# Kernel optimization log

Hardware: AMD Instinct MI355X
Metric: run time of the kernel (lower is better)

Reference implementation:

```python
import jax, jax.numpy as jnp
import numpy as np

N = {'QENT': 20000, 'CENT': 50000, 'SPAN': 40000, 'SENT': 40000}
E = 250000
IN_DIM, HID = 256, 128
NEG_SLOPE = 0.2  # GATConv default negative_slope
RELS = [('QENT', 'SPAN'), ('QENT', 'SENT'), ('CENT', 'SENT'), ('SPAN', 'CENT'), ('CENT', 'CENT')]
ENAMES = ['e_qent_span', 'e_qent_sent', 'e_cent_sent', 'e_span_cent', 'e_cent_cooccur']


def setup_inputs() -> dict:
    key = jax.random.key(0)
    ks = jax.random.split(key, 20)
    inp = {}
    for i, t in enumerate(['QENT', 'CENT', 'SPAN', 'SENT']):
        inp['x_' + t] = jax.random.normal(ks[i], (N[t], IN_DIM), jnp.float32)
    for i, (nm, (s, d)) in enumerate(zip(ENAMES, RELS)):
        k1, k2 = jax.random.split(ks[4 + i])
        src = jax.random.randint(k1, (E,), 0, N[s])
        dst = jax.random.randint(k2, (E,), 0, N[d])
        inp[nm] = jnp.stack([src, dst]).astype(jnp.int32)
    inp['lin_W'] = jax.random.normal(ks[10], (4, IN_DIM, HID), jnp.float32) / np.sqrt(IN_DIM).astype(np.float32)
    inp['lin_b'] = jnp.zeros((4, HID), jnp.float32)
    inp['conv_Ws'] = jax.random.normal(ks[11], (2, 5, HID, HID), jnp.float32) / np.sqrt(HID).astype(np.float32)
    inp['conv_Wd'] = jax.random.normal(ks[12], (2, 5, HID, HID), jnp.float32) / np.sqrt(HID).astype(np.float32)
    inp['conv_as'] = jax.random.normal(ks[13], (2, 5, HID), jnp.float32) / np.sqrt(HID).astype(np.float32)
    inp['conv_ad'] = jax.random.normal(ks[14], (2, 5, HID), jnp.float32) / np.sqrt(HID).astype(np.float32)
    inp['conv_b'] = jnp.zeros((2, 5, HID), jnp.float32)
    inp['out_W'] = jax.random.normal(ks[15], (HID, 1), jnp.float32) / np.sqrt(HID).astype(np.float32)
    inp['out_b'] = jnp.zeros((1,), jnp.float32)
    return inp


def _gat(x_src, x_dst, edge, Ws, Wd, a_s, a_d, b, n_dst):
    """PyG GATConv, heads=1, concat=True, add_self_loops=False, bipartite lin_src/lin_dst."""
    hs = x_src @ Ws                       # [Ns, H]
    hd = x_dst @ Wd                       # [Nd, H]
    src, dst = edge[0], edge[1]
    e = jax.nn.leaky_relu((hs @ a_s)[src] + (hd @ a_d)[dst], NEG_SLOPE)  # [E]
    m = jax.ops.segment_max(e, dst, num_segments=n_dst)
    m = jnp.where(jnp.isfinite(m), m, 0.0)
    ex = jnp.exp(e - m[dst])
    denom = jax.ops.segment_sum(ex, dst, num_segments=n_dst)
    alpha = ex / (denom[dst] + 1e-16)     # segment softmax (PyG adds 1e-16)
    out = jax.ops.segment_sum(alpha[:, None] * hs[src], dst, num_segments=n_dst)
    return out + b


def _forward(x_QENT, x_CENT, x_SPAN, x_SENT,
             e_qent_span, e_qent_sent, e_cent_sent, e_span_cent, e_cent_cooccur,
             lin_W, lin_b, conv_Ws, conv_Wd, conv_as, conv_ad, conv_b, out_W, out_b):
    # per-type input projection (pyg Linear has bias)
    x = {'QENT': x_QENT @ lin_W[0] + lin_b[0],
         'CENT': x_CENT @ lin_W[1] + lin_b[1],
         'SPAN': x_SPAN @ lin_W[2] + lin_b[2],
         'SENT': x_SENT @ lin_W[3] + lin_b[3]}
    for l in range(2):
        p = lambda r: (conv_Ws[l, r], conv_Wd[l, r], conv_as[l, r], conv_ad[l, r], conv_b[l, r])
        span = _gat(x['QENT'], x['SPAN'], e_qent_span, *p(0), N['SPAN'])
        sent = (_gat(x['QENT'], x['SENT'], e_qent_sent, *p(1), N['SENT'])
                + _gat(x['CENT'], x['SENT'], e_cent_sent, *p(2), N['SENT']))  # HeteroConv aggr='sum'
        cent = (_gat(x['SPAN'], x['CENT'], e_span_cent, *p(3), N['CENT'])
                + _gat(x['CENT'], x['CENT'], e_cent_cooccur, *p(4), N['CENT']))
        x = {'QENT': x['QENT'],  # QENT has no incoming edges; carried through so layer 2 can use it as source
             'SPAN': jax.nn.relu(span),
             'SENT': jax.nn.relu(sent),
             'CENT': jax.nn.relu(cent)}
    return (x['SPAN'] @ out_W + out_b)[:, 0]  # squeeze(-1) -> [N_SPAN]


def reference(x_QENT, x_CENT, x_SPAN, x_SENT,
              e_qent_span, e_qent_sent, e_cent_sent, e_span_cent, e_cent_cooccur,
              lin_W, lin_b, conv_Ws, conv_Wd, conv_as, conv_ad, conv_b, out_W, out_b):
    return _forward(x_QENT, x_CENT, x_SPAN, x_SENT,
                    e_qent_span, e_qent_sent, e_cent_sent, e_span_cent, e_cent_cooccur,
                    lin_W, lin_b, conv_Ws, conv_Wd, conv_as, conv_ad, conv_b, out_W, out_b)
```

## Files before the change

### kernel.cpp

```cpp
#include <hip/hip_runtime.h>
#include <hip/hip_fp16.h>

#define IN_DIM 256
#define HID 128
#define ELLW 16
#define OVF_CAP 32768

using bf16x8 = __attribute__((ext_vector_type(8))) short;
using f32x4 = __attribute__((ext_vector_type(4))) float;

struct h8 { __half2 a, b, c, d; };

__device__ __forceinline__ unsigned short f2bf(float f) {
    unsigned u = __float_as_uint(f);
    u += 0x7fffu + ((u >> 16) & 1u);
    return (unsigned short)(u >> 16);
}

template <int CTRL>
__device__ __forceinline__ float dpp_rot(float x) {
    return __int_as_float(
        __builtin_amdgcn_update_dpp(0, __float_as_int(x), CTRL, 0xf, 0xf, false));
}
__device__ __forceinline__ float rsum16(float x) {
    x += dpp_rot<0x121>(x);
    x += dpp_rot<0x122>(x);
    x += dpp_rot<0x124>(x);
    x += dpp_rot<0x128>(x);
    return x;
}
__device__ __forceinline__ float rmax16(float x) {
    x = fmaxf(x, dpp_rot<0x121>(x));
    x = fmaxf(x, dpp_rot<0x122>(x));
    x = fmaxf(x, dpp_rot<0x124>(x));
    x = fmaxf(x, dpp_rot<0x128>(x));
    return x;
}

__device__ __forceinline__ float lrelu(float t) { return t > 0.f ? t : 0.2f * t; }

__device__ __forceinline__ void accum8(f32x4& a0, f32x4& a1, float a, const h8& hv) {
    const float2 f0 = __half22float2(hv.a);
    const float2 f1 = __half22float2(hv.b);
    const float2 f2 = __half22float2(hv.c);
    const float2 f3 = __half22float2(hv.d);
    a0[0] += a * f0.x; a0[1] += a * f0.y;
    a0[2] += a * f1.x; a0[3] += a * f1.y;
    a1[0] += a * f2.x; a1[1] += a * f2.y;
    a1[2] += a * f3.x; a1[3] += a * f3.y;
}

__device__ __forceinline__ float epilogue16(const f32x4& a0, const f32x4& a1,
                                            const float* __restrict__ bias,
                                            const float* __restrict__ dvec, int sl) {
    const f32x4 bb0 = *reinterpret_cast<const f32x4*>(bias + sl * 8);
    const f32x4 bb1 = *reinterpret_cast<const f32x4*>(bias + sl * 8 + 4);
    const f32x4 d0 = *reinterpret_cast<const f32x4*>(dvec + sl * 8);
    const f32x4 d1 = *reinterpret_cast<const f32x4*>(dvec + sl * 8 + 4);
    float q = 0.f;
#pragma unroll
    for (int i = 0; i < 4; ++i) {
        q += fmaxf(a0[i] + bb0[i], 0.f) * d0[i];
        q += fmaxf(a1[i] + bb1[i], 0.f) * d1[i];
    }
    return rsum16(q);
}

__global__ __launch_bounds__(256) void setup_k(const float* __restrict__ lin_W,
                                               const float* __restrict__ lin_b,
                                               const float* __restrict__ conv_Ws,
                                               const float* __restrict__ Wd,
                                               const float* __restrict__ adv,
                                               short* __restrict__ wt0,
                                               short* __restrict__ wt1,
                                               float* __restrict__ bc,
                                               float* __restrict__ wd_out,
                                               float* __restrict__ v2,
                                               float* __restrict__ c2,
                                               int* __restrict__ deg,
                                               int* __restrict__ ovf_cnt, int NS) {
    const int b = blockIdx.x;
    if (b < 256) {
        const int idx = b * 256 + threadIdx.x;
        const int l = idx >> 15;
        const int rem = idx & 32767;
        const int k = rem >> 7;
        const int n = rem & 127;
        const float* lw = lin_W + (size_t)k * HID;
        const float* cw = conv_Ws + (size_t)(l * 5) * HID * HID + n;
        float s = 0.f;
#pragma unroll 4
        for (int m = 0; m < HID; ++m) s += lw[m] * cw[(size_t)m * HID];
        short* wt = l ? wt1 : wt0;
        wt[((k >> 3) << 10) + (n << 3) + (k & 7)] = (short)f2bf(s);
    } else if (b == 256) {
        const int t = threadIdx.x;
        const int l = t >> 7;
        const int n = t & 127;
        const float* cw = conv_Ws + (size_t)(l * 5) * HID * HID + n;
        float s = 0.f;
#pragma unroll 4
        for (int m = 0; m < HID; ++m) s += lin_b[m] * cw[(size_t)m * HID];
        bc[t] = s;
        if (t == 0) ovf_cnt[0] = 0;
    } else if (b == 257) {
        __shared__ float wd1s[HID];
        const int t = threadIdx.x;
        const int l = t >> 7, j = t & 127;
        const float* w = Wd + ((size_t)(l * 5) * HID + j) * HID;
        const float* a = adv + (size_t)(l * 5) * HID;
        float s = 0.f;
        for (int k = 0; k < HID; k += 4) {
            const float4 wv = *reinterpret_cast<const float4*>(w + k);
            const float4 av = *reinterpret_cast<const float4*>(a + k);
            s += wv.x * av.x + wv.y * av.y + wv.z * av.z + wv.w * av.w;
        }
        wd_out[t] = s;
        if (l == 0) wd1s[j] = s;
        __syncthreads();
        const float* wr = lin_W + 2 * (size_t)IN_DIM * HID + (size_t)t * HID;
        float p = 0.f;
        for (int k = 0; k < HID; k += 4) {
            const float4 wv = *reinterpret_cast<const float4*>(wr + k);
            p += wv.x * wd1s[k] + wv.y * wd1s[k + 1] + wv.z * wd1s[k + 2] +
                 wv.w * wd1s[k + 3];
        }
        v2[t] = p;
        if (t == 0) {
            const float* br = lin_b + 2 * HID;
            float q = 0.f;
            for (int k = 0; k < HID; ++k) q += br[k] * wd1s[k];
            c2[0] = q;
        }
    } else {
        const int i4 = ((b - 258) * 256 + threadIdx.x) * 4;
        if (i4 + 4 <= NS) {
            *reinterpret_cast<int4*>(deg + i4) = make_int4(0, 0, 0, 0);
        } else {
            for (int i = i4; i < NS; ++i) deg[i] = 0;
        }
    }
}

__global__ __launch_bounds__(256) void build_gemm_k(
    const int* __restrict__ src, const int* __restrict__ dst, int E,
    int* __restrict__ deg, int* __restrict__ ell, int2* __restrict__ ovf,
    int* __restrict__ ovf_cnt, const float* __restrict__ A,
    const short* __restrict__ Wt0, const short* __restrict__ Wt1,
    const float* __restrict__ bc, __half* __restrict__ hs,
    float2* __restrict__ as12, const float* __restrict__ a1v,
    const float* __restrict__ a2v, int N, int eb,
    const float* __restrict__ x_span, const float* __restrict__ v2,
    const float* __restrict__ c2, float* __restrict__ ad1_out, int NS, int gb) {
    if ((int)blockIdx.x < eb) {
        const int e = blockIdx.x * 256 + threadIdx.x;
        if (e < E) {
            const int d = dst[e], s = src[e];
            const int pos = atomicAdd(deg + d, 1);
            if (pos < ELLW) {
                ell[(size_t)d * ELLW + pos] = s;
            } else {
                const int oi = atomicAdd(ovf_cnt, 1);
                if (oi < OVF_CAP) ovf[oi] = make_int2(d, s);
            }
        }
        return;
    }
    if ((int)blockIdx.x >= eb + gb) {
        const int idx = ((int)blockIdx.x - eb - gb) * 256 + threadIdx.x;
        const int row = idx >> 4;
        const int sl = threadIdx.x & 15;
        if (row >= NS) return;
        const float* xr = x_span + (size_t)row * IN_DIM + sl * 16;
        const float* vr = v2 + sl * 16;
        float p = 0.f;
#pragma unroll
        for (int i = 0; i < 4; ++i) {
            const float4 xv = *reinterpret_cast<const float4*>(xr + i * 4);
            const float4 vv = *reinterpret_cast<const float4*>(vr + i * 4);
            p += xv.x * vv.x + xv.y * vv.y + xv.z * vv.z + xv.w * vv.w;
        }
        p = rsum16(p);
        if (sl == 0) ad1_out[row] = p + c2[0];
        return;
    }
    const int bid = (int)blockIdx.x - eb;
    const int tid = threadIdx.x;
    const int w = tid >> 6;
    const int lane = tid & 63;
    const int m16 = lane & 15;
    const int kg = lane >> 4;

    const int arow = bid * 64 + w * 16 + m16;
    const bool ok = arow < N;

    f32x4 acc[16];
#pragma unroll
    for (int j = 0; j < 16; ++j) acc[j] = (f32x4){0.f, 0.f, 0.f, 0.f};

    for (int k0 = 0; k0 < IN_DIM; k0 += 32) {
        bf16x8 af = {0, 0, 0, 0, 0, 0, 0, 0};
        if (ok) {
            const float* ap = A + (size_t)arow * IN_DIM + k0 + kg * 8;
            const float4 f0 = *reinterpret_cast<const float4*>(ap);
            const float4 f1 = *reinterpret_cast<const float4*>(ap + 4);
            af[0] = (short)f2bf(f0.x); af[1] = (short)f2bf(f0.y);
            af[2] = (short)f2bf(f0.z); af[3] = (short)f2bf(f0.w);
            af[4] = (short)f2bf(f1.x); af[5] = (short)f2bf(f1.y);
            af[6] = (short)f2bf(f1.z); af[7] = (short)f2bf(f1.w);
        }
        const int boff = ((k0 >> 3) + kg) << 10;
        const short* b0 = Wt0 + boff;
        const short* b1 = Wt1 + boff;
#pragma unroll
        for (int j = 0; j < 8; ++j) {
            const bf16x8 bf0 = *reinterpret_cast<const bf16x8*>(b0 + ((j * 16 + m16) << 3));
            acc[j] = __builtin_amdgcn_mfma_f32_16x16x32_bf16(af, bf0, acc[j], 0, 0, 0);
            const bf16x8 bf1 = *reinterpret_cast<const bf16x8*>(b1 + ((j * 16 + m16) << 3));
            acc[j + 8] = __builtin_amdgcn_mfma_f32_16x16x32_bf16(af, bf1, acc[j + 8], 0, 0, 0);
        }
    }

    const int rbase = bid * 64 + w * 16 + kg * 4;
    float p1[4] = {0.f, 0.f, 0.f, 0.f};
    float p2[4] = {0.f, 0.f, 0.f, 0.f};
#pragma unroll
    for (int j = 0; j < 8; ++j) {
        const int col = j * 16 + m16;
        const float b0v = bc[col];
        const float b1v = bc[128 + col];
        const float a1 = a1v[col];
        const float a2 = a2v[col];
        const int so = j * 32 + ((m16 >> 3) << 4) + (m16 & 7);
#pragma unroll
        for (int r = 0; r < 4; ++r) {
            const int row = rbase + r;
            const float v1 = acc[j][r] + b0v;
            const float v2v = acc[j + 8][r] + b1v;
            if (row < N) {
                hs[(size_t)row * 256 + so] = __float2half(v1);
                hs[(size_t)row * 256 + so + 8] = __float2half(v2v);
            }
            p1[r] += v1 * a1;
            p2[r] += v2v * a2;
        }
    }
#pragma unroll
    for (int r = 0; r < 4; ++r) {
        p1[r] = rsum16(p1[r]);
        p2[r] = rsum16(p2[r]);
    }
    if (m16 == 0)
#pragma unroll
        for (int r = 0; r < 4; ++r) {
            const int row = rbase + r;
            if (row < N) as12[row] = make_float2(p1[r], p2[r]);
        }
}

__global__ __launch_bounds__(256, 4) void gat_fused_k(
    const int* __restrict__ deg_arr, const int* __restrict__ ell,
    const int2* __restrict__ ovf, const int* __restrict__ ovf_cnt_p,
    const float* __restrict__ ad1_arr, const float2* __restrict__ as12,
    const __half* __restrict__ hs, const float* __restrict__ b1,
    const float* __restrict__ wd2v, const float* __restrict__ b2,
    const float* __restrict__ outW, const float* __restrict__ outb,
    float* __restrict__ out, int Ndst) {
    const int row = (blockIdx.x * blockDim.x + threadIdx.x) >> 6;
    const int lane = threadIdx.x & 63;
    const int sl = lane & 15;
    const int eg = lane >> 4;
    if (row >= Ndst) return;

    const int deg = deg_arr[row];
    int ce = ell[(size_t)row * ELLW + sl];
    if (sl >= deg) ce = 0;
    const float2 asv = as12[ce];
    const float ad1 = ad1_arr[row];

    if (deg <= ELLW) {
        const float ex1 = (sl < deg) ? __expf(lrelu(asv.x + ad1)) : 0.f;
        const float al1 = ex1 / (rsum16(ex1) + 1e-16f);

        f32x4 a0 = {0.f, 0.f, 0.f, 0.f}, a1 = {0.f, 0.f, 0.f, 0.f};
        h8 h2s[4];
#pragma unroll
        for (int r = 0; r < 4; ++r) {
            if (r * 4 < deg) {
                const int e = r * 4 + eg;
                const int s = __shfl(ce, e, 64);
                const float a = __shfl(al1, e, 64);
                const __half* hb = hs + (size_t)s * 256 + sl * 16;
                const h8 hv1 = *reinterpret_cast<const h8*>(hb);
                h2s[r] = *reinterpret_cast<const h8*>(hb + 8);
                accum8(a0, a1, a, hv1);
            }
        }
#pragma unroll
        for (int i = 0; i < 4; ++i) {
            a0[i] += __shfl_xor(a0[i], 16, 64);
            a0[i] += __shfl_xor(a0[i], 32, 64);
            a1[i] += __shfl_xor(a1[i], 16, 64);
            a1[i] += __shfl_xor(a1[i], 32, 64);
        }
        const float ad2 = epilogue16(a0, a1, b1, wd2v, sl);

        const float ex2 = (sl < deg) ? __expf(lrelu(asv.y + ad2)) : 0.f;
        const float al2 = ex2 / (rsum16(ex2) + 1e-16f);

        f32x4 b0 = {0.f, 0.f, 0.f, 0.f}, b1v = {0.f, 0.f, 0.f, 0.f};
#pragma unroll
        for (int r = 0; r < 4; ++r) {
            if (r * 4 < deg) {
                const float a = __shfl(al2, r * 4 + eg, 64);
                accum8(b0, b1v, a, h2s[r]);
            }
        }
#pragma unroll
        for (int i = 0; i < 4; ++i) {
            b0[i] += __shfl_xor(b0[i], 16, 64);
            b0[i] += __shfl_xor(b0[i], 32, 64);
            b1v[i] += __shfl_xor(b1v[i], 16, 64);
            b1v[i] += __shfl_xor(b1v[i], 32, 64);
        }
        const float q = epilogue16(b0, b1v, b2, outW, sl);
        if (lane == 0) out[row] = q + outb[0];
    } else {
        int oc = *ovf_cnt_p;
        if (oc > OVF_CAP) oc = OVF_CAP;
        float ad = ad1;
#pragma unroll
        for (int layer = 0; layer < 2; ++layer) {
            const float ac = layer ? asv.y : asv.x;
            const int ho = layer ? 8 : 0;
            const float* bias = layer ? b2 : b1;
            const float* dvec = layer ? outW : wd2v;

            float te = lrelu(ac + ad);
            float m = rmax16(te);
            for (int i = 0; i < oc; ++i) {
                const int2 o = ovf[i];
                if (o.x == row) {
                    const float2 oas = as12[o.y];
                    m = fmaxf(m, lrelu((layer ? oas.y : oas.x) + ad));
                }
            }
            const float ex = __expf(te - m);
            float dsum = rsum16(ex);
            for (int i = 0; i < oc; ++i) {
                const int2 o = ovf[i];
                if (o.x == row) {
                    const float2 oas = as12[o.y];
                    dsum += __expf(lrelu((layer ? oas.y : oas.x) + ad) - m);
                }
            }
            const float inv = 1.f / (dsum + 1e-16f);
            const float al = ex * inv;

            f32x4 acc0 = {0.f, 0.f, 0.f, 0.f}, acc1 = {0.f, 0.f, 0.f, 0.f};
            for (int i = 0; i < 16; ++i) {
                const int s = __shfl(ce, i, 64);
                float a = __shfl(al, i, 64);
                if (eg != 0) a = 0.f;
                const h8 hv =
                    *reinterpret_cast<const h8*>(hs + (size_t)s * 256 + sl * 16 + ho);
                accum8(acc0, acc1, a, hv);
            }
            for (int i = 0; i < oc; ++i) {
                const int2 o = ovf[i];
                if (o.x == row && eg == 0) {
                    const float2 oas = as12[o.y];
                    const float a = __expf(lrelu((layer ? oas.y : oas.x) + ad) - m) * inv;
                    const h8 hv =
                        *reinterpret_cast<const h8*>(hs + (size_t)o.y * 256 + sl * 16 + ho);
                    accum8(acc0, acc1, a, hv);
                }
            }
#pragma unroll
            for (int i = 0; i < 4; ++i) {
                acc0[i] += __shfl_xor(acc0[i], 16, 64);
                acc0[i] += __shfl_xor(acc0[i], 32, 64);
                acc1[i] += __shfl_xor(acc1[i], 16, 64);
                acc1[i] += __shfl_xor(acc1[i], 32, 64);
            }
            const float q = epilogue16(acc0, acc1, bias, dvec, sl);
            if (layer == 0) {
                ad = q;
            } else if (lane == 0) {
                out[row] = q + outb[0];
            }
        }
    }
}

extern "C" void kernel_launch(void* const* d_in, const int* in_sizes, int n_in,
                              void* d_out, int out_size, void* d_ws, size_t ws_size,
                              hipStream_t stream) {
    const float* x_qent = (const float*)d_in[0];
    const float* x_span = (const float*)d_in[2];
    const int* e_qs = (const int*)d_in[4];
    const float* lin_W = (const float*)d_in[9];
    const float* lin_b = (const float*)d_in[10];
    const float* conv_Ws = (const float*)d_in[11];
    const float* conv_Wd = (const float*)d_in[12];
    const float* conv_as = (const float*)d_in[13];
    const float* conv_ad = (const float*)d_in[14];
    const float* conv_b = (const float*)d_in[15];
    const float* out_W = (const float*)d_in[16];
    const float* out_b = (const float*)d_in[17];

    const int NQ = in_sizes[0] / IN_DIM;
    const int NS = in_sizes[2] / IN_DIM;
    const int E = in_sizes[4] / 2;
    const int* srcp = e_qs;
    const int* dstp = e_qs + E;
    (void)n_in; (void)out_size;

    float* ws = (float*)d_ws;
    size_t off = 0;
    auto alloc = [&](size_t n) {
        n = (n + 3) & ~(size_t)3;
        float* p = ws + off;
        off += n;
        return p;
    };
    __half* hs = (__half*)alloc((size_t)NQ * 128);
    float2* as12 = (float2*)alloc(2 * (size_t)NQ);
    float* ad1 = alloc(NS);
    float* wd2 = alloc(2 * HID);
    float* v2 = alloc(IN_DIM);
    float* c2 = alloc(1);
    float* bc = alloc(2 * HID);
    int* deg = (int*)alloc(NS);
    int* ell = (int*)alloc((size_t)NS * ELLW);
    int2* ovf = (int2*)alloc(2 * OVF_CAP);
    int* ovf_cnt = (int*)alloc(1);
    short* wt0 = (short*)alloc(IN_DIM * HID / 2);
    short* wt1 = (short*)alloc(IN_DIM * HID / 2);
    (void)ws_size;

    const int zd = (NS + 1023) / 1024;
    setup_k<<<dim3(258 + zd), dim3(256), 0, stream>>>(
        lin_W, lin_b, conv_Ws, conv_Wd, conv_ad, wt0, wt1, bc, wd2, v2, c2, deg, ovf_cnt,
        NS);

    const int eb = (E + 255) / 256;
    const int gb = (NQ + 63) / 64;
    const int ab = ((size_t)NS * 16 + 255) / 256;
    build_gemm_k<<<dim3(eb + gb + ab), dim3(256), 0, stream>>>(
        srcp, dstp, E, deg, ell, ovf, ovf_cnt, x_qent, wt0, wt1, bc, hs, as12, conv_as,
        conv_as + 5 * (size_t)HID, NQ, eb, x_span, v2, c2, ad1, NS, gb);

    gat_fused_k<<<dim3(((size_t)NS * 64 + 255) / 256), dim3(256), 0, stream>>>(
        deg, ell, ovf, ovf_cnt, ad1, as12, hs, conv_b, wd2 + HID,
        conv_b + 5 * (size_t)HID, out_W, out_b, (float*)d_out, NS);
}
```

Measured before the change: 85.60 us.

## Split GEMM blocks per weight matrix and reorder fused-kernel block roles

Each GEMM block previously computed both 128-wide projections (16 accumulators). It now computes one projection, selected by block-index parity, which doubles the GEMM block count and halves the accumulator registers per block. The block order inside the fused kernel also changes so GEMM blocks launch first, then the ad1 dot-product blocks, then the edge-scatter blocks, so the heavy work starts early. The trade-off is that each A row is read and converted to bf16 twice, and the two halves of the attention-score pair are now written by separate blocks as scalar stores.

```diff
diff --git a/kernel.cpp b/kernel.cpp
--- a/kernel.cpp
+++ b/kernel.cpp
@@ -148,26 +148,78 @@
     int* __restrict__ ovf_cnt, const float* __restrict__ A,
     const short* __restrict__ Wt0, const short* __restrict__ Wt1,
     const float* __restrict__ bc, __half* __restrict__ hs,
-    float2* __restrict__ as12, const float* __restrict__ a1v,
-    const float* __restrict__ a2v, int N, int eb,
+    float* __restrict__ as12,
+    const float* __restrict__ a1v, const float* __restrict__ a2v, int N,
     const float* __restrict__ x_span, const float* __restrict__ v2,
-    const float* __restrict__ c2, float* __restrict__ ad1_out, int NS, int gb) {
-    if ((int)blockIdx.x < eb) {
-        const int e = blockIdx.x * 256 + threadIdx.x;
-        if (e < E) {
-            const int d = dst[e], s = src[e];
-            const int pos = atomicAdd(deg + d, 1);
-            if (pos < ELLW) {
-                ell[(size_t)d * ELLW + pos] = s;
-            } else {
-                const int oi = atomicAdd(ovf_cnt, 1);
-                if (oi < OVF_CAP) ovf[oi] = make_int2(d, s);
-            }
-        }
+    const float* __restrict__ c2, float* __restrict__ ad1_out, int NS, int gb2,
+    int ab) {
+    const int b = (int)blockIdx.x;
+    if (b < gb2) {
+        const int l = b & 1;
+        const int bid = b >> 1;
+        const short* Wt = l ? Wt1 : Wt0;
+        const float* av = l ? a2v : a1v;
+        const int tid = threadIdx.x;
+        const int w = tid >> 6;
+        const int lane = tid & 63;
+        const int m16 = lane & 15;
+        const int kg = lane >> 4;
+
+        const int arow = bid * 64 + w * 16 + m16;
+        const bool ok = arow < N;
+
+        f32x4 acc[8];
+#pragma unroll
+        for (int j = 0; j < 8; ++j) acc[j] = (f32x4){0.f, 0.f, 0.f, 0.f};
+
+        for (int k0 = 0; k0 < IN_DIM; k0 += 32) {
+            bf16x8 af = {0, 0, 0, 0, 0, 0, 0, 0};
+            if (ok) {
+                const float* ap = A + (size_t)arow * IN_DIM + k0 + kg * 8;
+                const float4 f0 = *reinterpret_cast<const float4*>(ap);
+                const float4 f1 = *reinterpret_cast<const float4*>(ap + 4);
+                af[0] = (short)f2bf(f0.x); af[1] = (short)f2bf(f0.y);
+                af[2] = (short)f2bf(f0.z); af[3] = (short)f2bf(f0.w);
+                af[4] = (short)f2bf(f1.x); af[5] = (short)f2bf(f1.y);
+                af[6] = (short)f2bf(f1.z); af[7] = (short)f2bf(f1.w);
+            }
+            const short* bbase = Wt + (((k0 >> 3) + kg) << 10);
+#pragma unroll
+            for (int j = 0; j < 8; ++j) {
+                const bf16x8 bf =
+                    *reinterpret_cast<const bf16x8*>(bbase + ((j * 16 + m16) << 3));
+                acc[j] = __builtin_amdgcn_mfma_f32_16x16x32_bf16(af, bf, acc[j], 0, 0, 0);
+            }
+        }
+
+        const int rbase = bid * 64 + w * 16 + kg * 4;
+        float p[4] = {0.f, 0.f, 0.f, 0.f};
+#pragma unroll
+        for (int j = 0; j < 8; ++j) {
+            const int col = j * 16 + m16;
+            const float bv = bc[l * 128 + col];
+            const float a = av[col];
+            const int so = j * 32 + ((m16 >> 3) << 4) + (m16 & 7) + l * 8;
+#pragma unroll
+            for (int r = 0; r < 4; ++r) {
+                const int row = rbase + r;
+                const float v = acc[j][r] + bv;
+                if (row < N) hs[(size_t)row * 256 + so] = __float2half(v);
+                p[r] += v * a;
+            }
+        }
+#pragma unroll
+        for (int r = 0; r < 4; ++r) p[r] = rsum16(p[r]);
+        if (m16 == 0)
+#pragma unroll
+            for (int r = 0; r < 4; ++r) {
+                const int row = rbase + r;
+                if (row < N) as12[2 * (size_t)row + l] = p[r];
+            }
         return;
     }
-    if ((int)blockIdx.x >= eb + gb) {
-        const int idx = ((int)blockIdx.x - eb - gb) * 256 + threadIdx.x;
+    if (b < gb2 + ab) {
+        const int idx = (b - gb2) * 256 + threadIdx.x;
         const int row = idx >> 4;
         const int sl = threadIdx.x & 15;
         if (row >= NS) return;
@@ -184,78 +236,17 @@
         if (sl == 0) ad1_out[row] = p + c2[0];
         return;
     }
-    const int bid = (int)blockIdx.x - eb;
-    const int tid = threadIdx.x;
-    const int w = tid >> 6;
-    const int lane = tid & 63;
-    const int m16 = lane & 15;
-    const int kg = lane >> 4;
-
-    const int arow = bid * 64 + w * 16 + m16;
-    const bool ok = arow < N;
-
-    f32x4 acc[16];
-#pragma unroll
-    for (int j = 0; j < 16; ++j) acc[j] = (f32x4){0.f, 0.f, 0.f, 0.f};
-
-    for (int k0 = 0; k0 < IN_DIM; k0 += 32) {
-        bf16x8 af = {0, 0, 0, 0, 0, 0, 0, 0};
-        if (ok) {
-            const float* ap = A + (size_t)arow * IN_DIM + k0 + kg * 8;
-            const float4 f0 = *reinterpret_cast<const float4*>(ap);
-            const float4 f1 = *reinterpret_cast<const float4*>(ap + 4);
-            af[0] = (short)f2bf(f0.x); af[1] = (short)f2bf(f0.y);
-            af[2] = (short)f2bf(f0.z); af[3] = (short)f2bf(f0.w);
-            af[4] = (short)f2bf(f1.x); af[5] = (short)f2bf(f1.y);
-            af[6] = (short)f2bf(f1.z); af[7] = (short)f2bf(f1.w);
-        }
-        const int boff = ((k0 >> 3) + kg) << 10;
-        const short* b0 = Wt0 + boff;
-        const short* b1 = Wt1 + boff;
-#pragma unroll
-        for (int j = 0; j < 8; ++j) {
-            const bf16x8 bf0 = *reinterpret_cast<const bf16x8*>(b0 + ((j * 16 + m16) << 3));
-            acc[j] = __builtin_amdgcn_mfma_f32_16x16x32_bf16(af, bf0, acc[j], 0, 0, 0);
-            const bf16x8 bf1 = *reinterpret_cast<const bf16x8*>(b1 + ((j * 16 + m16) << 3));
-            acc[j + 8] = __builtin_amdgcn_mfma_f32_16x16x32_bf16(af, bf1, acc[j + 8], 0, 0, 0);
-        }
-    }
-
-    const int rbase = bid * 64 + w * 16 + kg * 4;
-    float p1[4] = {0.f, 0.f, 0.f, 0.f};
-    float p2[4] = {0.f, 0.f, 0.f, 0.f};
-#pragma unroll
-    for (int j = 0; j < 8; ++j) {
-        const int col = j * 16 + m16;
-        const float b0v = bc[col];
-        const float b1v = bc[128 + col];
-        const float a1 = a1v[col];
-        const float a2 = a2v[col];
-        const int so = j * 32 + ((m16 >> 3) << 4) + (m16 & 7);
-#pragma unroll
-        for (int r = 0; r < 4; ++r) {
-            const int row = rbase + r;
-            const float v1 = acc[j][r] + b0v;
-            const float v2v = acc[j + 8][r] + b1v;
-            if (row < N) {
-                hs[(size_t)row * 256 + so] = __float2half(v1);
-                hs[(size_t)row * 256 + so + 8] = __float2half(v2v);
-            }
-            p1[r] += v1 * a1;
-            p2[r] += v2v * a2;
-        }
-    }
-#pragma unroll
-    for (int r = 0; r < 4; ++r) {
-        p1[r] = rsum16(p1[r]);
-        p2[r] = rsum16(p2[r]);
-    }
-    if (m16 == 0)
-#pragma unroll
-        for (int r = 0; r < 4; ++r) {
-            const int row = rbase + r;
-            if (row < N) as12[row] = make_float2(p1[r], p2[r]);
-        }
+    const int e = (b - gb2 - ab) * 256 + threadIdx.x;
+    if (e < E) {
+        const int d = dst[e], s = src[e];
+        const int pos = atomicAdd(deg + d, 1);
+        if (pos < ELLW) {
+            ell[(size_t)d * ELLW + pos] = s;
+        } else {
+            const int oi = atomicAdd(ovf_cnt, 1);
+            if (oi < OVF_CAP) ovf[oi] = make_int2(d, s);
+        }
+    }
 }
 
 __global__ __launch_bounds__(256, 4) void gat_fused_k(
@@ -425,7 +416,7 @@
         return p;
     };
     __half* hs = (__half*)alloc((size_t)NQ * 128);
-    float2* as12 = (float2*)alloc(2 * (size_t)NQ);
+    float* as12 = alloc(2 * (size_t)NQ);
     float* ad1 = alloc(NS);
     float* wd2 = alloc(2 * HID);
     float* v2 = alloc(IN_DIM);
@@ -444,14 +435,14 @@
         lin_W, lin_b, conv_Ws, conv_Wd, conv_ad, wt0, wt1, bc, wd2, v2, c2, deg, ovf_cnt,
         NS);
 
+    const int gb2 = 2 * ((NQ + 63) / 64);
+    const int ab = ((size_t)NS * 16 + 255) / 256;
     const int eb = (E + 255) / 256;
-    const int gb = (NQ + 63) / 64;
-    const int ab = ((size_t)NS * 16 + 255) / 256;
-    build_gemm_k<<<dim3(eb + gb + ab), dim3(256), 0, stream>>>(
+    build_gemm_k<<<dim3(gb2 + ab + eb), dim3(256), 0, stream>>>(
         srcp, dstp, E, deg, ell, ovf, ovf_cnt, x_qent, wt0, wt1, bc, hs, as12, conv_as,
-        conv_as + 5 * (size_t)HID, NQ, eb, x_span, v2, c2, ad1, NS, gb);
+        conv_as + 5 * (size_t)HID, NQ, x_span, v2, c2, ad1, NS, gb2, ab);
 
     gat_fused_k<<<dim3(((size_t)NS * 64 + 255) / 256), dim3(256), 0, stream>>>(
-        deg, ell, ovf, ovf_cnt, ad1, as12, hs, conv_b, wd2 + HID,
+        deg, ell, ovf, ovf_cnt, ad1, (const float2*)as12, hs, conv_b, wd2 + HID,
         conv_b + 5 * (size_t)HID, out_W, out_b, (float*)d_out, NS);
 }
```

New measurement: 81.60 us, median of 2. 1.05x faster.
